# Kernel optimization log

Hardware: AMD Instinct MI355X
Metric: run time of the kernel (lower is better)

Reference implementation:

```python
import jax, jax.numpy as jnp
import numpy as np

B, T, C = 4, 2048, 2048
N_HEAD, N_HEAD_KV = 16, 4
HEAD_DIM = C // N_HEAD
ROPE_BASE = 10000.0


def setup_inputs() -> dict:
    key = jax.random.key(0)
    ks = jax.random.split(key, 6)
    x = jax.random.normal(ks[0], (B, T, C), dtype=jnp.float32)
    # freqs_cis: (T, head_dim//2, 2) with [...,0]=cos, [...,1]=sin (true RoPE angles)
    inv_freq = 1.0 / (ROPE_BASE ** (jnp.arange(0, HEAD_DIM, 2, dtype=jnp.float32) / HEAD_DIM))
    angles = jnp.arange(T, dtype=jnp.float32)[:, None] * inv_freq[None, :]  # (T, hd//2)
    freqs_cis = jnp.stack([jnp.cos(angles), jnp.sin(angles)], axis=-1)
    s = 0.02
    Wq = jax.random.normal(ks[1], (C, C), dtype=jnp.float32) * s
    Wk = jax.random.normal(ks[2], (N_HEAD_KV * HEAD_DIM, C), dtype=jnp.float32) * s
    Wv = jax.random.normal(ks[3], (N_HEAD_KV * HEAD_DIM, C), dtype=jnp.float32) * s
    Wo = jax.random.normal(ks[4], (C, C), dtype=jnp.float32) * s
    return {"x": x, "freqs_cis": freqs_cis, "Wq": Wq, "Wk": Wk, "Wv": Wv, "Wo": Wo}


def _rotate_half(u):
    h = u.shape[-1] // 2
    return jnp.concatenate([-u[..., h:], u[..., :h]], axis=-1)


def reference(x, freqs_cis, Wq, Wk, Wv, Wo):
    b, t, c = x.shape
    hd = HEAD_DIM
    q = (x @ Wq.T).reshape(b, t, N_HEAD, hd)
    k = (x @ Wk.T).reshape(b, t, N_HEAD_KV, hd)
    v = (x @ Wv.T).reshape(b, t, N_HEAD_KV, hd)
    # external RoPE (3-dim freqs_cis): cos/sin repeated to full head_dim
    cos = freqs_cis[:t, :, 0]
    sin = freqs_cis[:t, :, 1]
    cos = jnp.concatenate([cos, cos], axis=-1)[None, :, None, :]  # (1,T,1,hd)
    sin = jnp.concatenate([sin, sin], axis=-1)[None, :, None, :]
    q = q * cos + _rotate_half(q) * sin
    k = k * cos + _rotate_half(k) * sin
    # GQA: repeat_interleave kv heads to n_head
    g = N_HEAD // N_HEAD_KV
    k = jnp.repeat(k, g, axis=2)  # (B,T,H,hd)
    v = jnp.repeat(v, g, axis=2)
    scale = 1.0 / np.sqrt(hd)
    scores = jnp.einsum('bthd,bshd->bhts', q, k) * scale  # (B,H,T,S)
    causal = jnp.tril(jnp.ones((t, t), dtype=bool))
    neg = jnp.finfo(scores.dtype).min
    scores = jnp.where(causal[None, None, :, :], scores, neg)
    attn = jax.nn.softmax(scores, axis=-1)
    out = jnp.einsum('bhts,bshd->bthd', attn, v).reshape(b, t, c)
    return out @ Wo.T
```

## Files before the change

### kernel.cpp

```cpp
#include <hip/hip_runtime.h>
#include <hip/hip_bf16.h>
#include <stdint.h>

typedef __bf16 bf16_t;
typedef __bf16 bf16x4 __attribute__((ext_vector_type(4)));
typedef __bf16 bf16x8 __attribute__((ext_vector_type(8)));
typedef float f32x4 __attribute__((ext_vector_type(4)));

__device__ __forceinline__ float fast_exp2(float x) {
#if __has_builtin(__builtin_amdgcn_exp2f)
  return __builtin_amdgcn_exp2f(x);
#else
  return exp2f(x);
#endif
}

__global__ void cvt_all(const float* __restrict__ x,  const float* __restrict__ Wq,
                        const float* __restrict__ Wk, const float* __restrict__ Wv,
                        const float* __restrict__ Wo, bf16_t* __restrict__ xb,
                        bf16_t* __restrict__ wqkv, bf16_t* __restrict__ wob) {
  const int bid = blockIdx.x, tid = threadIdx.x;
  const float* src; bf16_t* dst; int i;
  if (bid < 16384)      { src = x;  dst = xb;             i = bid * 256 + tid; }
  else if (bid < 20480) { src = Wq; dst = wqkv;           i = (bid - 16384) * 256 + tid; }
  else if (bid < 21504) { src = Wk; dst = wqkv + 4194304; i = (bid - 20480) * 256 + tid; }
  else if (bid < 22528) { src = Wv; dst = wqkv + 5242880; i = (bid - 21504) * 256 + tid; }
  else                  { src = Wo; dst = wob;            i = (bid - 22528) * 256 + tid; }
  float4 v = ((const float4*)src)[i];
  bf16x4 o = { (bf16_t)v.x, (bf16_t)v.y, (bf16_t)v.z, (bf16_t)v.w };
  *(bf16x4*)(dst + (size_t)i * 4) = o;
}

__device__ __forceinline__ void async_load16(const bf16_t* g, bf16_t* l) {
#if __has_builtin(__builtin_amdgcn_global_load_lds)
  __builtin_amdgcn_global_load_lds((const __attribute__((address_space(1))) void*)g,
                                   (__attribute__((address_space(3))) void*)l, 16, 0, 0);
#else
  *(bf16x8*)l = *(const bf16x8*)g;
#endif
}

template<bool F32OUT, bool VSPLIT>
__global__ __launch_bounds__(512, 2) void gemm256(const bf16_t* __restrict__ A,
                                                  const bf16_t* __restrict__ B,
                                                  void* __restrict__ C,
                                                  bf16_t* __restrict__ Vt,
                                                  int NBN, int K, int ldc) {
  __shared__ bf16_t As[2][256 * 64];
  __shared__ bf16_t Bs[2][256 * 64];
  const int tid = threadIdx.x;
  const int wave = tid >> 6, lane = tid & 63;
  const int lrow = lane & 15, quad = lane >> 4;
  const int wr = wave >> 2, wc = wave & 3;
  const int nwg = gridDim.x;
  const int wg  = (blockIdx.x & 7) * (nwg >> 3) + (blockIdx.x >> 3);
  const int bm = wg / NBN, bn = wg % NBN;
  const bf16_t* Ag = A + (size_t)bm * 256 * K;
  const bf16_t* Bg = B + (size_t)bn * 256 * K;
  const int srow = tid >> 3;
  const int schunk = (tid & 7) ^ (srow & 7);

  f32x4 acc[2][2][4][2] = {};
  bf16x8 af[4][2], bfr[2][2];
  const int NT = K >> 6;

  auto stageA = [&](int mh, int bsel, int kk) {
#pragma unroll
    for (int i = 0; i < 2; ++i)
      async_load16(Ag + (size_t)(mh * 128 + i * 64 + srow) * K + kk + schunk * 8,
                   &As[bsel][mh * 8192 + i * 4096 + tid * 8]);
  };
  auto stageB = [&](int nh, int bsel, int kk) {
#pragma unroll
    for (int i = 0; i < 2; ++i)
      async_load16(Bg + (size_t)(nh * 128 + i * 64 + srow) * K + kk + schunk * 8,
                   &Bs[bsel][nh * 8192 + i * 4096 + tid * 8]);
  };

#define READ_A(MH)                                                                   \
  _Pragma("unroll")                                                                  \
  for (int mfi = 0; mfi < 4; ++mfi) {                                                \
    const int ra = (MH) * 128 + mfi * 32 + wr * 16 + lrow;                           \
    _Pragma("unroll")                                                                \
    for (int ks = 0; ks < 2; ++ks)                                                   \
      af[mfi][ks] = *(const bf16x8*)&As[buf][ra * 64 +                               \
                        (((ks * 4 + quad) ^ (lrow & 7)) << 3)];                      \
  }
#define READ_B(NH)                                                                   \
  _Pragma("unroll")                                                                  \
  for (int nfi = 0; nfi < 2; ++nfi) {                                                \
    const int rb = (NH) * 128 + nfi * 64 + wc * 16 + lrow;                           \
    _Pragma("unroll")                                                                \
    for (int ks = 0; ks < 2; ++ks)                                                   \
      bfr[nfi][ks] = *(const bf16x8*)&Bs[buf][rb * 64 +                              \
                         (((ks * 4 + quad) ^ (lrow & 7)) << 3)];                     \
  }
#define MFMA_Q(MH, NH)                                                               \
  __builtin_amdgcn_s_setprio(1);                                                     \
  _Pragma("unroll")                                                                  \
  for (int ks = 0; ks < 2; ++ks)                                                     \
    _Pragma("unroll")                                                                \
    for (int mfi = 0; mfi < 4; ++mfi)                                                \
      _Pragma("unroll")                                                              \
      for (int nfi = 0; nfi < 2; ++nfi)                                              \
        acc[MH][NH][mfi][nfi] = __builtin_amdgcn_mfma_f32_16x16x32_bf16(             \
            af[mfi][ks], bfr[nfi][ks], acc[MH][NH][mfi][nfi], 0, 0, 0);              \
  __builtin_amdgcn_s_setprio(0);

  stageA(0, 0, 0);
  stageB(0, 0, 0);
  stageB(1, 0, 0);
  stageA(1, 0, 0);
  asm volatile("s_waitcnt vmcnt(4)" ::: "memory");
  __builtin_amdgcn_s_barrier();

  for (int t = 0; t < NT; ++t) {
    const int buf = t & 1, obuf = buf ^ 1;
    const int kn = (t + 1) << 6;
    const bool pf = (t + 1 < NT);
    READ_A(0)
    READ_B(0)
    if (pf) stageA(0, obuf, kn);
    __builtin_amdgcn_s_barrier();
    asm volatile("s_waitcnt lgkmcnt(0)" ::: "memory");
    MFMA_Q(0, 0)
    if (pf) asm volatile("s_waitcnt vmcnt(4)" ::: "memory");
    else    asm volatile("s_waitcnt vmcnt(2)" ::: "memory");
    __builtin_amdgcn_s_barrier();
    READ_B(1)
    if (pf) stageB(0, obuf, kn);
    __builtin_amdgcn_s_barrier();
    asm volatile("s_waitcnt lgkmcnt(0)" ::: "memory");
    MFMA_Q(0, 1)
    if (pf) asm volatile("s_waitcnt vmcnt(4)" ::: "memory");
    else    asm volatile("s_waitcnt vmcnt(0)" ::: "memory");
    __builtin_amdgcn_s_barrier();
    READ_A(1)
    if (pf) stageB(1, obuf, kn);
    __builtin_amdgcn_s_barrier();
    asm volatile("s_waitcnt lgkmcnt(0)" ::: "memory");
    MFMA_Q(1, 1)
    __builtin_amdgcn_s_barrier();
    READ_B(0)
    if (pf) stageA(1, obuf, kn);
    __builtin_amdgcn_s_barrier();
    asm volatile("s_waitcnt lgkmcnt(0)" ::: "memory");
    MFMA_Q(1, 0)
    if (pf) asm volatile("s_waitcnt vmcnt(4)" ::: "memory");
    __builtin_amdgcn_s_barrier();
  }
#undef READ_A
#undef READ_B
#undef MFMA_Q

  if (VSPLIT && bn >= 10) {
#pragma unroll
    for (int mh = 0; mh < 2; ++mh)
#pragma unroll
      for (int nh = 0; nh < 2; ++nh)
#pragma unroll
        for (int mfi = 0; mfi < 4; ++mfi)
#pragma unroll
          for (int nfi = 0; nfi < 2; ++nfi) {
            int row = bm * 256 + mh * 128 + mfi * 32 + wr * 16 + quad * 4;
            int cv  = bn * 256 + nh * 128 + nfi * 64 + wc * 16 + lrow - 2560;
            int b = row >> 11, tl = row & 2047;
            bf16x4 o;
#pragma unroll
            for (int r = 0; r < 4; ++r) o[r] = (bf16_t)acc[mh][nh][mfi][nfi][r];
            *(bf16x4*)&Vt[((size_t)(b * 512 + cv)) * 2048 + tl] = o;
          }
    return;
  }
#pragma unroll
  for (int mh = 0; mh < 2; ++mh)
#pragma unroll
    for (int nh = 0; nh < 2; ++nh)
#pragma unroll
      for (int mfi = 0; mfi < 4; ++mfi)
#pragma unroll
        for (int nfi = 0; nfi < 2; ++nfi)
#pragma unroll
          for (int r = 0; r < 4; ++r) {
            int row = bm * 256 + mh * 128 + mfi * 32 + wr * 16 + quad * 4 + r;
            int col = bn * 256 + nh * 128 + nfi * 64 + wc * 16 + lrow;
            if (F32OUT) ((float*)C)[(size_t)row * ldc + col] = acc[mh][nh][mfi][nfi][r];
            else        ((bf16_t*)C)[(size_t)row * ldc + col] = (bf16_t)acc[mh][nh][mfi][nfi][r];
          }
}

__global__ void rope_kernel(bf16_t* __restrict__ X, const float* __restrict__ F,
                            int hshift, int stride) {
  int i = blockIdx.x * blockDim.x + threadIdx.x;
  int d = i & 63;
  int h = (i >> 6) & ((1 << hshift) - 1);
  int row = i >> (6 + hshift);
  int t = row & 2047;
  float c = F[t * 128 + d * 2];
  float s = F[t * 128 + d * 2 + 1];
  size_t base = (size_t)row * stride + h * 128 + d;
  float q0 = (float)X[base];
  float q1 = (float)X[base + 64];
  X[base]      = (bf16_t)(q0 * c - q1 * s);
  X[base + 64] = (bf16_t)(q1 * c + q0 * s);
}

__global__ __launch_bounds__(256, 2) void attn_kernel(const bf16_t* __restrict__ QKV,
                                                      const float* __restrict__ F,
                                                      const bf16_t* __restrict__ Vt,
                                                      bf16_t* __restrict__ O) {
  __shared__ bf16_t Ks[2][64 * 128];
  __shared__ bf16_t Vs[2][128 * 64];
  __shared__ bf16_t Ps[4 * 32 * 64];
  const int tid = threadIdx.x;
  const int wave = tid >> 6, lane = tid & 63;
  const int lrow = lane & 15, quad = lane >> 4;
  const int bh = blockIdx.y, b = bh >> 4, h = bh & 15, kvh = h >> 2;
  const size_t qoff  = ((size_t)b * 2048) * 2560 + (size_t)h * 128;
  const size_t koff  = ((size_t)b * 2048) * 2560 + 2048 + (size_t)kvh * 128;
  const size_t vtoff = ((size_t)(b * 4 + kvh) * 128) * 2048;
  const float qsc = 0.08838834764831845f * 1.44269504088896340736f;
  bf16_t* Pw = Ps + wave * (32 * 64);
  const float2* F2 = (const float2*)F;

  const int krow_l = tid >> 4;
  const int kdc    = (tid & 15) ^ (krow_l & 7);
  const int vrow_l = tid >> 3;
  const int vkc    = (tid & 7) ^ (vrow_l & 7);

  auto stage = [&](int kt, int bsel) {
    const bf16_t* Kg = QKV + koff + (size_t)(kt * 64) * 2560;
    const bf16_t* Vg = Vt + vtoff + kt * 64;
    bf16_t* Kd = &Ks[bsel][0];
    bf16_t* Vd = &Vs[bsel][0];
#pragma unroll
    for (int c4 = 0; c4 < 4; ++c4) {
      int ci = c4 * 256 + tid;
      async_load16(Kg + (size_t)(c4 * 16 + krow_l) * 2560 + kdc * 8, Kd + ci * 8);
      async_load16(Vg + (size_t)(c4 * 32 + vrow_l) * 2048 + vkc * 8, Vd + ci * 8);
    }
  };

  for (int phase = 0; phase < 2; ++phase) {
    const int qt = phase ? (15 - blockIdx.x) : blockIdx.x;
    const int qbase = qt * 128 + wave * 32;

    bf16x8 qf[2][4];
#pragma unroll
    for (int nt2 = 0; nt2 < 2; ++nt2) {
      const int t = qbase + nt2 * 16 + lrow;
      const bf16_t* qp = QKV + qoff + (size_t)t * 2560 + quad * 8;
      bf16x8 raw[4];
#pragma unroll
      for (int ks = 0; ks < 4; ++ks) raw[ks] = *(const bf16x8*)(qp + ks * 32);
#pragma unroll
      for (int ks2 = 0; ks2 < 2; ++ks2) {
        bf16x8 lo, hi;
#pragma unroll
        for (int j = 0; j < 8; ++j) {
          int d = ks2 * 32 + quad * 8 + j;
          float2 cs = F2[t * 64 + d];
          float q0 = (float)raw[ks2][j], q1 = (float)raw[ks2 + 2][j];
          lo[j] = (bf16_t)((q0 * cs.x - q1 * cs.y) * qsc);
          hi[j] = (bf16_t)((q1 * cs.x + q0 * cs.y) * qsc);
        }
        qf[nt2][ks2]     = lo;
        qf[nt2][ks2 + 2] = hi;
      }
    }

    f32x4 Oacc[2][8] = {};
    float m_r[2] = {-1.0e30f, -1.0e30f};
    float l_r[2] = {0.f, 0.f};
    const int kt_end = 2 * qt + 2;

    stage(0, 0);

    for (int kt = 0; kt < kt_end; ++kt) {
      __syncthreads();
      if (kt + 1 < kt_end) stage(kt + 1, (kt + 1) & 1);
      const bf16_t* Kb_ = &Ks[kt & 1][0];
      const bf16_t* Vb_ = &Vs[kt & 1][0];

      if (kt * 64 <= qbase + 31) {
        f32x4 S[2][4] = {};
#pragma unroll
        for (int ks = 0; ks < 4; ++ks) {
          bf16x8 kf[4];
#pragma unroll
          for (int mt = 0; mt < 4; ++mt) {
            int dc = (ks * 4 + quad) ^ (lrow & 7);
            kf[mt] = *(const bf16x8*)&Kb_[(mt * 16 + lrow) * 128 + dc * 8];
          }
#pragma unroll
          for (int nt2 = 0; nt2 < 2; ++nt2)
#pragma unroll
            for (int mt = 0; mt < 4; ++mt)
              S[nt2][mt] = __builtin_amdgcn_mfma_f32_16x16x32_bf16(kf[mt], qf[nt2][ks], S[nt2][mt], 0, 0, 0);
        }
        if (kt * 64 + 63 > qbase) {
#pragma unroll
          for (int nt2 = 0; nt2 < 2; ++nt2) {
            int q = qbase + nt2 * 16 + lrow;
#pragma unroll
            for (int mt = 0; mt < 4; ++mt) {
              int key0 = kt * 64 + mt * 16 + quad * 4;
#pragma unroll
              for (int r = 0; r < 4; ++r)
                if (key0 + r > q) S[nt2][mt][r] = -1.0e30f;
            }
          }
        }
        float alpha[2];
#pragma unroll
        for (int nt2 = 0; nt2 < 2; ++nt2) {
          float mx = -1.0e30f;
#pragma unroll
          for (int mt = 0; mt < 4; ++mt)
#pragma unroll
            for (int r = 0; r < 4; ++r) mx = fmaxf(mx, S[nt2][mt][r]);
          mx = fmaxf(mx, __shfl_xor(mx, 16, 64));
          mx = fmaxf(mx, __shfl_xor(mx, 32, 64));
          float mnew = fmaxf(m_r[nt2], mx);
          alpha[nt2] = fast_exp2(m_r[nt2] - mnew);
          m_r[nt2] = mnew;
          float rs = 0.f;
          const int prow = nt2 * 16 + lrow;
          const int pbase = prow * 64 + ((quad & 1) << 2);
#pragma unroll
          for (int mt = 0; mt < 4; ++mt) {
            bf16x4 pk;
#pragma unroll
            for (int r = 0; r < 4; ++r) {
              float p = fast_exp2(S[nt2][mt][r] - mnew);
              rs += p;
              pk[r] = (bf16_t)p;
            }
            int c8 = ((mt * 2 + (quad >> 1)) ^ (prow & 7)) << 3;
            *(bf16x4*)&Pw[pbase + c8] = pk;
          }
          rs += __shfl_xor(rs, 16, 64);
          rs += __shfl_xor(rs, 32, 64);
          l_r[nt2] = l_r[nt2] * alpha[nt2] + rs;
        }
        bool nz = (alpha[0] != 1.f) || (alpha[1] != 1.f);
        if (__ballot(nz) != 0ull) {
#pragma unroll
          for (int mt2 = 0; mt2 < 2; ++mt2)
#pragma unroll
            for (int r = 0; r < 4; ++r) {
              float av = __shfl(alpha[mt2], quad * 4 + r, 16);
#pragma unroll
              for (int dt = 0; dt < 8; ++dt) Oacc[mt2][dt][r] *= av;
            }
        }
#pragma unroll
        for (int ks2 = 0; ks2 < 2; ++ks2) {
          bf16x8 ap[2];
#pragma unroll
          for (int mt2 = 0; mt2 < 2; ++mt2) {
            int prow = mt2 * 16 + lrow;
            ap[mt2] = *(const bf16x8*)&Pw[prow * 64 + (((ks2 * 4 + quad) ^ (prow & 7)) << 3)];
          }
          int dc = (ks2 * 4 + quad) ^ (lrow & 7);
#pragma unroll
          for (int dt = 0; dt < 8; ++dt) {
            bf16x8 bv = *(const bf16x8*)&Vb_[(dt * 16 + lrow) * 64 + dc * 8];
#pragma unroll
            for (int mt2 = 0; mt2 < 2; ++mt2)
              Oacc[mt2][dt] = __builtin_amdgcn_mfma_f32_16x16x32_bf16(ap[mt2], bv, Oacc[mt2][dt], 0, 0, 0);
          }
        }
      }
    }

#pragma unroll
    for (int mt2 = 0; mt2 < 2; ++mt2)
#pragma unroll
      for (int r = 0; r < 4; ++r) {
        float lv = __shfl(l_r[mt2], quad * 4 + r, 16);
        float inv = 1.0f / lv;
        int row = qbase + mt2 * 16 + quad * 4 + r;
#pragma unroll
        for (int dt = 0; dt < 8; ++dt)
          O[(size_t)b * 2048 * 2048 + (size_t)row * 2048 + h * 128 + dt * 16 + lrow] =
              (bf16_t)(Oacc[mt2][dt][r] * inv);
      }
  }
}

extern "C" void kernel_launch(void* const* d_in, const int* in_sizes, int n_in,
                              void* d_out, int out_size, void* d_ws, size_t ws_size,
                              hipStream_t stream) {
  const float* x  = (const float*)d_in[0];
  const float* fc = (const float*)d_in[1];
  const float* Wq = (const float*)d_in[2];
  const float* Wk = (const float*)d_in[3];
  const float* Wv = (const float*)d_in[4];
  const float* Wo = (const float*)d_in[5];
  float* out = (float*)d_out;

  char* ws = (char*)d_ws;
  size_t off = 0;
  auto alloc = [&](size_t bytes) { char* p = ws + off; off += bytes; return p; };
  bf16_t* xb    = (bf16_t*)alloc((size_t)8192 * 2048 * 2);
  bf16_t* Wqkvb = (bf16_t*)alloc((size_t)3072 * 2048 * 2);
  bf16_t* Wob   = (bf16_t*)alloc((size_t)2048 * 2048 * 2);
  bf16_t* QKVb  = (bf16_t*)alloc((size_t)8192 * 2560 * 2);
  bf16_t* Ab    = (bf16_t*)alloc((size_t)8192 * 2048 * 2);
  bf16_t* Vtb   = (bf16_t*)alloc((size_t)2048 * 2048 * 2);
  (void)ws_size; (void)in_sizes; (void)n_in; (void)out_size;

  cvt_all<<<26624, 256, 0, stream>>>(x, Wq, Wk, Wv, Wo, xb, Wqkvb, Wob);

  gemm256<false, true><<<384, 512, 0, stream>>>(xb, Wqkvb, QKVb, Vtb, 12, 2048, 2560);

  rope_kernel<<<8192, 256, 0, stream>>>(QKVb + 2048, fc, 2, 2560);

  attn_kernel<<<dim3(8, 64), 256, 0, stream>>>(QKVb, fc, Vtb, Ab);

  gemm256<true, false><<<256, 512, 0, stream>>>(Ab, Wob, out, nullptr, 8, 2048, 2048);
}
```

Before: 463.2 us.

## Use 256x128 GEMM tiles for QKV projection and lazy softmax max rescaling

Adds a GEMM variant with 256x128 output tiles (8 waves in a 4x2 layout) for the QKV projection. This doubles the grid to 768 workgroups so the 256 CUs are loaded more evenly than with 384 large tiles. It also changes the attention softmax to keep the old running max unless the new max exceeds it by more than 8 (log2 units), which skips rescaling work. The cost is less operand reuse per tile and a small extra risk of precision loss from unrescaled exponentials.

```diff
diff --git a/kernel.cpp b/kernel.cpp
--- a/kernel.cpp
+++ b/kernel.cpp
@@ -38,6 +38,153 @@
 #else
   *(bf16x8*)l = *(const bf16x8*)g;
 #endif
+}
+
+template<bool F32OUT, bool VSPLIT>
+__global__ __launch_bounds__(512, 2) void gemm_bal(const bf16_t* __restrict__ A,
+                                                   const bf16_t* __restrict__ B,
+                                                   void* __restrict__ C,
+                                                   bf16_t* __restrict__ Vt,
+                                                   int NBN, int K, int ldc) {
+  __shared__ bf16_t As[2][256 * 64];
+  __shared__ bf16_t Bs[2][128 * 64];
+  const int tid = threadIdx.x;
+  const int wave = tid >> 6, lane = tid & 63;
+  const int lrow = lane & 15, quad = lane >> 4;
+  const int wr = wave >> 1, wc = wave & 1;
+  const int nwg = gridDim.x;
+  const int wg  = (blockIdx.x & 7) * (nwg >> 3) + (blockIdx.x >> 3);
+  const int bm = wg / NBN, bn = wg % NBN;
+  const bf16_t* Ag = A + (size_t)bm * 256 * K;
+  const bf16_t* Bg = B + (size_t)bn * 128 * K;
+  const int srow = tid >> 3;
+  const int schunk = (tid & 7) ^ (srow & 7);
+
+  f32x4 acc[2][2][2][2] = {};
+  bf16x8 af[2][2], bfr[2][2];
+  const int NT = K >> 6;
+
+  auto stageA = [&](int mh, int bsel, int kk) {
+#pragma unroll
+    for (int i = 0; i < 2; ++i)
+      async_load16(Ag + (size_t)(mh * 128 + i * 64 + srow) * K + kk + schunk * 8,
+                   &As[bsel][mh * 8192 + i * 4096 + tid * 8]);
+  };
+  auto stageB = [&](int nh, int bsel, int kk) {
+    async_load16(Bg + (size_t)(nh * 64 + srow) * K + kk + schunk * 8,
+                 &Bs[bsel][nh * 4096 + tid * 8]);
+  };
+
+#define READ_A(MH)                                                                   \
+  _Pragma("unroll")                                                                  \
+  for (int mfi = 0; mfi < 2; ++mfi) {                                                \
+    const int ra = (MH) * 128 + mfi * 64 + wr * 16 + lrow;                           \
+    _Pragma("unroll")                                                                \
+    for (int ks = 0; ks < 2; ++ks)                                                   \
+      af[mfi][ks] = *(const bf16x8*)&As[buf][ra * 64 +                               \
+                        (((ks * 4 + quad) ^ (lrow & 7)) << 3)];                      \
+  }
+#define READ_B(NH)                                                                   \
+  _Pragma("unroll")                                                                  \
+  for (int nfi = 0; nfi < 2; ++nfi) {                                                \
+    const int rb = (NH) * 64 + nfi * 32 + wc * 16 + lrow;                            \
+    _Pragma("unroll")                                                                \
+    for (int ks = 0; ks < 2; ++ks)                                                   \
+      bfr[nfi][ks] = *(const bf16x8*)&Bs[buf][rb * 64 +                              \
+                         (((ks * 4 + quad) ^ (lrow & 7)) << 3)];                     \
+  }
+#define MFMA_Q(MH, NH)                                                               \
+  __builtin_amdgcn_s_setprio(1);                                                     \
+  _Pragma("unroll")                                                                  \
+  for (int ks = 0; ks < 2; ++ks)                                                     \
+    _Pragma("unroll")                                                                \
+    for (int mfi = 0; mfi < 2; ++mfi)                                                \
+      _Pragma("unroll")                                                              \
+      for (int nfi = 0; nfi < 2; ++nfi)                                              \
+        acc[MH][NH][mfi][nfi] = __builtin_amdgcn_mfma_f32_16x16x32_bf16(             \
+            af[mfi][ks], bfr[nfi][ks], acc[MH][NH][mfi][nfi], 0, 0, 0);              \
+  __builtin_amdgcn_s_setprio(0);
+
+  stageA(0, 0, 0);
+  stageB(0, 0, 0);
+  stageB(1, 0, 0);
+  stageA(1, 0, 0);
+  asm volatile("s_waitcnt vmcnt(3)" ::: "memory");
+  __builtin_amdgcn_s_barrier();
+
+  for (int t = 0; t < NT; ++t) {
+    const int buf = t & 1, obuf = buf ^ 1;
+    const int kn = (t + 1) << 6;
+    const bool pf = (t + 1 < NT);
+    READ_A(0)
+    READ_B(0)
+    if (pf) stageA(0, obuf, kn);
+    __builtin_amdgcn_s_barrier();
+    asm volatile("s_waitcnt lgkmcnt(0)" ::: "memory");
+    MFMA_Q(0, 0)
+    if (pf) asm volatile("s_waitcnt vmcnt(4)" ::: "memory");
+    else    asm volatile("s_waitcnt vmcnt(2)" ::: "memory");
+    __builtin_amdgcn_s_barrier();
+    READ_B(1)
+    if (pf) stageB(0, obuf, kn);
+    __builtin_amdgcn_s_barrier();
+    asm volatile("s_waitcnt lgkmcnt(0)" ::: "memory");
+    MFMA_Q(0, 1)
+    if (pf) asm volatile("s_waitcnt vmcnt(3)" ::: "memory");
+    else    asm volatile("s_waitcnt vmcnt(0)" ::: "memory");
+    __builtin_amdgcn_s_barrier();
+    READ_A(1)
+    if (pf) stageB(1, obuf, kn);
+    __builtin_amdgcn_s_barrier();
+    asm volatile("s_waitcnt lgkmcnt(0)" ::: "memory");
+    MFMA_Q(1, 1)
+    __builtin_amdgcn_s_barrier();
+    READ_B(0)
+    if (pf) stageA(1, obuf, kn);
+    __builtin_amdgcn_s_barrier();
+    asm volatile("s_waitcnt lgkmcnt(0)" ::: "memory");
+    MFMA_Q(1, 0)
+    if (pf) asm volatile("s_waitcnt vmcnt(3)" ::: "memory");
+    __builtin_amdgcn_s_barrier();
+  }
+#undef READ_A
+#undef READ_B
+#undef MFMA_Q
+
+  if (VSPLIT && bn >= 20) {
+#pragma unroll
+    for (int mh = 0; mh < 2; ++mh)
+#pragma unroll
+      for (int nh = 0; nh < 2; ++nh)
+#pragma unroll
+        for (int mfi = 0; mfi < 2; ++mfi)
+#pragma unroll
+          for (int nfi = 0; nfi < 2; ++nfi) {
+            int row = bm * 256 + mh * 128 + mfi * 64 + wr * 16 + quad * 4;
+            int cv  = bn * 128 + nh * 64 + nfi * 32 + wc * 16 + lrow - 2560;
+            int b = row >> 11, tl = row & 2047;
+            bf16x4 o;
+#pragma unroll
+            for (int r = 0; r < 4; ++r) o[r] = (bf16_t)acc[mh][nh][mfi][nfi][r];
+            *(bf16x4*)&Vt[((size_t)(b * 512 + cv)) * 2048 + tl] = o;
+          }
+    return;
+  }
+#pragma unroll
+  for (int mh = 0; mh < 2; ++mh)
+#pragma unroll
+    for (int nh = 0; nh < 2; ++nh)
+#pragma unroll
+      for (int mfi = 0; mfi < 2; ++mfi)
+#pragma unroll
+        for (int nfi = 0; nfi < 2; ++nfi)
+#pragma unroll
+          for (int r = 0; r < 4; ++r) {
+            int row = bm * 256 + mh * 128 + mfi * 64 + wr * 16 + quad * 4 + r;
+            int col = bn * 128 + nh * 64 + nfi * 32 + wc * 16 + lrow;
+            if (F32OUT) ((float*)C)[(size_t)row * ldc + col] = acc[mh][nh][mfi][nfi][r];
+            else        ((bf16_t*)C)[(size_t)row * ldc + col] = (bf16_t)acc[mh][nh][mfi][nfi][r];
+          }
 }
 
 template<bool F32OUT, bool VSPLIT>
@@ -321,8 +468,9 @@
             for (int r = 0; r < 4; ++r) mx = fmaxf(mx, S[nt2][mt][r]);
           mx = fmaxf(mx, __shfl_xor(mx, 16, 64));
           mx = fmaxf(mx, __shfl_xor(mx, 32, 64));
-          float mnew = fmaxf(m_r[nt2], mx);
-          alpha[nt2] = fast_exp2(m_r[nt2] - mnew);
+          float mold = m_r[nt2];
+          float mnew = (mx - mold <= 8.0f) ? mold : mx;
+          alpha[nt2] = fast_exp2(mold - mnew);
           m_r[nt2] = mnew;
           float rs = 0.f;
           const int prow = nt2 * 16 + lrow;
@@ -413,7 +561,7 @@
 
   cvt_all<<<26624, 256, 0, stream>>>(x, Wq, Wk, Wv, Wo, xb, Wqkvb, Wob);
 
-  gemm256<false, true><<<384, 512, 0, stream>>>(xb, Wqkvb, QKVb, Vtb, 12, 2048, 2560);
+  gemm_bal<false, true><<<768, 512, 0, stream>>>(xb, Wqkvb, QKVb, Vtb, 24, 2048, 2560);
 
   rope_kernel<<<8192, 256, 0, stream>>>(QKVb + 2048, fc, 2, 2560);
 
```

Result: no change. 459.9 us (-0.7%).
